# Optimization experiments

Measured on AMD Instinct MI355X. Metric: run time of the kernel, lower is better.

Reference implementation:

```python
import jax, jax.numpy as jnp
import numpy as np

B, N, DIM = 2, 2048, 2048
H, HD = 16, 128
EPS = 1e-5


def rmsnorm(x, w, eps=EPS):
    return x * jax.lax.rsqrt(jnp.mean(x * x, axis=-1, keepdims=True) + eps) * w


def rope(x, fr, fi):
    # x: [B, N, H, D]; fr/fi: [B, N, D//2] -> broadcast over heads
    x2 = x.reshape(*x.shape[:-1], HD // 2, 2)  # [B,N,H,D/2,2]
    x0, x1 = x2[..., 0], x2[..., 1]
    fr = fr[:, :, None, :]
    fi = fi[:, :, None, :]
    o0 = x0 * fr - x1 * fi
    o1 = x0 * fi + x1 * fr
    return jnp.stack([o0, o1], axis=-1).reshape(x.shape)


def setup_inputs() -> dict:
    key = jax.random.key(0)
    ks = jax.random.split(key, 7)
    s = 1.0 / np.sqrt(DIM)
    return {
        "x": jax.random.normal(ks[0], (B, N, DIM), jnp.float32),
        "freqs_real": jax.random.normal(ks[1], (B, N, HD // 2), jnp.float32),
        "freqs_imag": jax.random.normal(ks[2], (B, N, HD // 2), jnp.float32),
        "w_qkv": jax.random.normal(ks[3], (DIM, 3 * H * HD), jnp.float32) * s,
        "w_out": jax.random.normal(ks[4], (H * HD, DIM), jnp.float32) * s,
        "q_norm_w": jnp.ones((HD,), jnp.float32),
        "k_norm_w": jnp.ones((HD,), jnp.float32),
    }


def reference(x, freqs_real, freqs_imag, w_qkv, w_out, q_norm_w, k_norm_w):
    qkv = (x @ w_qkv).reshape(B, N, 3, H, HD)
    q, k, v = qkv[:, :, 0], qkv[:, :, 1], qkv[:, :, 2]  # [B,N,H,D]
    q = rmsnorm(q, q_norm_w)
    k = rmsnorm(k, k_norm_w)
    q = rope(q, freqs_real, freqs_imag)
    k = rope(k, freqs_real, freqs_imag)
    scale = 1.0 / np.sqrt(HD)
    scores = jnp.einsum("bqhd,bkhd->bhqk", q, k) * scale
    attn = jax.nn.softmax(scores, axis=-1)
    out = jnp.einsum("bhqk,bkhd->bqhd", attn, v).reshape(B, N, H * HD)
    return out @ w_out
```

## Files before the change

kernel.cpp:

```cpp
#include <hip/hip_runtime.h>
#include <hip/hip_bf16.h>
#include <stdint.h>

#define B_    2
#define N_    2048
#define DIM_  2048
#define H_    16
#define HD_   128
#define NH3   6144
#define ROWS  4096
#define EPS_  1e-5f

typedef unsigned short u16;
typedef __bf16 bf16x8 __attribute__((ext_vector_type(8)));
typedef float  f32x4  __attribute__((ext_vector_type(4)));

__device__ inline f32x4 mfma16(bf16x8 a, bf16x8 b, f32x4 c) {
  return __builtin_amdgcn_mfma_f32_16x16x32_bf16(a, b, c, 0, 0, 0);
}

__device__ inline u16 f2bf(float f) {
  union { float f; uint32_t u; } v; v.f = f;
  uint32_t u = v.u;
  return (u16)((u + 0x7fffu + ((u >> 16) & 1u)) >> 16);
}
__device__ inline float bf2f(u16 u) {
  union { uint32_t u; float f; } v; v.u = ((uint32_t)u) << 16;
  return v.f;
}

__device__ inline void gload_lds16(const void* g, void* l) {
  __builtin_amdgcn_global_load_lds(
      (const __attribute__((address_space(1))) void*)g,
      (__attribute__((address_space(3))) void*)l, 16, 0, 0);
}

__global__ __launch_bounds__(256) void cvt_f32_bf16(const float* __restrict__ in,
                                                    u16* __restrict__ out, int n) {
  int i = (blockIdx.x * 256 + threadIdx.x) * 4;
  if (i >= n) return;
  float4 v = *(const float4*)&in[i];
  ushort4 o;
  o.x = f2bf(v.x); o.y = f2bf(v.y); o.z = f2bf(v.z); o.w = f2bf(v.w);
  *(ushort4*)&out[i] = o;
}

__global__ __launch_bounds__(256) void transpose_cvt(const float* __restrict__ in,
                                                     u16* __restrict__ out,
                                                     int R, int C) {
  __shared__ float tile[32][33];
  int tc = blockIdx.x * 32, tr = blockIdx.y * 32;
  int tx = threadIdx.x, ty = threadIdx.y;
  #pragma unroll
  for (int i = 0; i < 4; ++i)
    tile[ty + i*8][tx] = in[(size_t)(tr + ty + i*8) * C + tc + tx];
  __syncthreads();
  #pragma unroll
  for (int i = 0; i < 4; ++i)
    out[(size_t)(tc + ty + i*8) * R + tr + tx] = f2bf(tile[tx][ty + i*8]);
}

__global__ __launch_bounds__(256) void v_transpose(const u16* __restrict__ qkv,
                                                   u16* __restrict__ vt) {
  __shared__ u16 lT[64][130];
  int bh = blockIdx.y, n0 = blockIdx.x * 64;
  int b = bh >> 4, h = bh & 15;
  int t = threadIdx.x;
  const u16* Vb = qkv + (size_t)b * N_ * NH3 + 4096 + h * HD_;
  #pragma unroll
  for (int i = 0; i < 16; ++i) {
    int chunk = i * 256 + t;
    int n = chunk >> 6, dc = chunk & 63;
    *(ushort2*)&lT[n][dc*2] = *(const ushort2*)&Vb[(size_t)(n0+n)*NH3 + dc*2];
  }
  __syncthreads();
  u16* vo = vt + (size_t)bh * HD_ * N_;
  #pragma unroll
  for (int i = 0; i < 4; ++i) {
    int chunk = i * 256 + t;
    int d = chunk >> 3, nc = chunk & 7;
    ushort4 a, bq;
    a.x = lT[nc*8+0][d]; a.y = lT[nc*8+1][d]; a.z = lT[nc*8+2][d]; a.w = lT[nc*8+3][d];
    bq.x = lT[nc*8+4][d]; bq.y = lT[nc*8+5][d]; bq.z = lT[nc*8+6][d]; bq.w = lT[nc*8+7][d];
    u16* dst = &vo[(size_t)d * N_ + n0 + nc*8];
    *(ushort4*)dst = a;
    *(ushort4*)(dst+4) = bq;
  }
}

template <bool OUT_BF16>
__global__ __launch_bounds__(256) void gemm_bt(const u16* __restrict__ A,
                                               const u16* __restrict__ Bt,
                                               void* __restrict__ Cv,
                                               int M, int N, int K) {
  __shared__ u16 lA[128][64];
  __shared__ u16 lB[128][64];
  int per = gridDim.x >> 3;
  int nid = (blockIdx.x & 7) * per + (blockIdx.x >> 3);
  int MB = M >> 7;
  int m0 = (nid % MB) * 128, n0 = (nid / MB) * 128;
  int t = threadIdx.x;
  int wave = t >> 6, lane = t & 63;
  int wr = wave >> 1, wc = wave & 1;
  int lhi = lane >> 4, llo = lane & 15;
  int lrow = lane >> 3, lcol = lane & 7;
  f32x4 acc[4][4] = {};

  for (int k0 = 0; k0 < K; k0 += 64) {
    __syncthreads();
    #pragma unroll
    for (int i = 0; i < 4; ++i) {
      int chunk = i * 4 + wave;
      int row = chunk * 8 + lrow;
      gload_lds16(&A[(size_t)(m0+row)*K + k0 + lcol*8], &lA[chunk*8][0]);
      gload_lds16(&Bt[(size_t)(n0+row)*K + k0 + lcol*8], &lB[chunk*8][0]);
    }
    __syncthreads();
    #pragma unroll
    for (int kk = 0; kk < 2; ++kk) {
      bf16x8 af[4], bfr[4];
      #pragma unroll
      for (int mi = 0; mi < 4; ++mi)
        af[mi] = *(const bf16x8*)&lA[wr*64 + mi*16 + llo][kk*32 + lhi*8];
      #pragma unroll
      for (int ni = 0; ni < 4; ++ni)
        bfr[ni] = *(const bf16x8*)&lB[wc*64 + ni*16 + llo][kk*32 + lhi*8];
      #pragma unroll
      for (int mi = 0; mi < 4; ++mi)
        #pragma unroll
        for (int ni = 0; ni < 4; ++ni)
          acc[mi][ni] = mfma16(af[mi], bfr[ni], acc[mi][ni]);
    }
  }
  #pragma unroll
  for (int mi = 0; mi < 4; ++mi)
    #pragma unroll
    for (int ni = 0; ni < 4; ++ni)
      #pragma unroll
      for (int r = 0; r < 4; ++r) {
        int row = m0 + wr*64 + mi*16 + lhi*4 + r;
        int col = n0 + wc*64 + ni*16 + llo;
        float v = acc[mi][ni][r];
        if constexpr (OUT_BF16) ((u16*)Cv)[(size_t)row*N + col] = f2bf(v);
        else                    ((float*)Cv)[(size_t)row*N + col] = v;
      }
}

__global__ __launch_bounds__(256) void norm_rope(u16* __restrict__ qkv,
                                                 const float* __restrict__ fr,
                                                 const float* __restrict__ fi,
                                                 const float* __restrict__ qw,
                                                 const float* __restrict__ kw) {
  int gw = (blockIdx.x * 256 + threadIdx.x) >> 6;
  int lane = threadIdx.x & 63;
  int row = gw >> 4, h = gw & 15;
  size_t base = (size_t)row * NH3 + h * HD_;
  ushort2 qp = *(ushort2*)&qkv[base + 2*lane];
  ushort2 kp = *(ushort2*)&qkv[base + 2048 + 2*lane];
  float q0 = bf2f(qp.x), q1 = bf2f(qp.y);
  float k0 = bf2f(kp.x), k1 = bf2f(kp.y);
  float sq = q0*q0 + q1*q1;
  float sk = k0*k0 + k1*k1;
  #pragma unroll
  for (int off = 1; off < 64; off <<= 1) {
    sq += __shfl_xor(sq, off);
    sk += __shfl_xor(sk, off);
  }
  float rq = rsqrtf(sq * (1.0f/128.0f) + EPS_);
  float rk = rsqrtf(sk * (1.0f/128.0f) + EPS_);
  float wq0 = qw[2*lane], wq1 = qw[2*lane+1];
  float wk0 = kw[2*lane], wk1 = kw[2*lane+1];
  q0 *= rq * wq0; q1 *= rq * wq1;
  k0 *= rk * wk0; k1 *= rk * wk1;
  float fre = fr[(size_t)row*64 + lane], fim = fi[(size_t)row*64 + lane];
  float qo0 = q0*fre - q1*fim, qo1 = q0*fim + q1*fre;
  float ko0 = k0*fre - k1*fim, ko1 = k0*fim + k1*fre;
  const float SC = 0.08838834764831845f;
  qo0 *= SC; qo1 *= SC;
  ushort2 qo, ko;
  qo.x = f2bf(qo0); qo.y = f2bf(qo1);
  ko.x = f2bf(ko0); ko.y = f2bf(ko1);
  *(ushort2*)&qkv[base + 2*lane] = qo;
  *(ushort2*)&qkv[base + 2048 + 2*lane] = ko;
}

__global__ __launch_bounds__(256) void attn(const u16* __restrict__ qkv,
                                            const u16* __restrict__ vt,
                                            u16* __restrict__ out) {
  int nid = (blockIdx.x & 7) * 64 + (blockIdx.x >> 3);
  int bh = nid >> 4;
  int b = bh >> 4, h = bh & 15;
  int q0 = (nid & 15) * 128;
  int t = threadIdx.x, wave = t >> 6, lane = t & 63;
  int lhi = lane >> 4, llo = lane & 15;

  __shared__ u16 lK[64][136];
  __shared__ u16 lVt[128][72];
  __shared__ u16 lP[4][32][72];

  const u16* Qb  = qkv + (size_t)b * N_ * NH3 + h * HD_;
  const u16* Kb  = Qb + 2048;
  const u16* Vtb = vt + (size_t)bh * HD_ * N_;

  bf16x8 qf[2][4];
  #pragma unroll
  for (int pi = 0; pi < 2; ++pi) {
    const u16* qrow = Qb + (size_t)(q0 + wave*32 + pi*16 + llo) * NH3;
    #pragma unroll
    for (int kk = 0; kk < 4; ++kk)
      qf[pi][kk] = *(const bf16x8*)&qrow[kk*32 + lhi*8];
  }

  f32x4 o[2][8] = {};
  float m_own[2] = {-1e30f, -1e30f};
  float l_own[2] = {0.f, 0.f};

  for (int kv0 = 0; kv0 < N_; kv0 += 64) {
    __syncthreads();
    #pragma unroll
    for (int i = 0; i < 4; ++i) {
      int chunk = i*256 + t;
      int row = chunk >> 4, kc = chunk & 15;
      *(int4*)&lK[row][kc*8] = *(const int4*)&Kb[(size_t)(kv0+row)*NH3 + kc*8];
    }
    #pragma unroll
    for (int i = 0; i < 4; ++i) {
      int chunk = i*256 + t;
      int d = chunk >> 3, kvc = chunk & 7;
      *(int4*)&lVt[d][kvc*8] = *(const int4*)&Vtb[(size_t)d*N_ + kv0 + kvc*8];
    }
    __syncthreads();

    f32x4 St[2][4];
    #pragma unroll
    for (int pi = 0; pi < 2; ++pi)
      #pragma unroll
      for (int j = 0; j < 4; ++j) St[pi][j] = f32x4{0.f,0.f,0.f,0.f};
    #pragma unroll
    for (int j = 0; j < 4; ++j)
      #pragma unroll
      for (int kk = 0; kk < 4; ++kk) {
        bf16x8 kf = *(const bf16x8*)&lK[j*16 + llo][kk*32 + lhi*8];
        St[0][j] = mfma16(kf, qf[0][kk], St[0][j]);
        St[1][j] = mfma16(kf, qf[1][kk], St[1][j]);
      }

    float scb[2][4];
    #pragma unroll
    for (int pi = 0; pi < 2; ++pi) {
      float mx = -1e30f;
      #pragma unroll
      for (int j = 0; j < 4; ++j) {
        float a = fmaxf(fmaxf(St[pi][j][0], St[pi][j][1]),
                        fmaxf(St[pi][j][2], St[pi][j][3]));
        mx = fmaxf(mx, a);
      }
      mx = fmaxf(mx, __shfl_xor(mx, 16));
      mx = fmaxf(mx, __shfl_xor(mx, 32));
      float mnew = fmaxf(m_own[pi], mx);
      float sc = __expf(m_own[pi] - mnew);
      m_own[pi] = mnew;
      float rs = 0.f;
      #pragma unroll
      for (int j = 0; j < 4; ++j)
        #pragma unroll
        for (int r = 0; r < 4; ++r) {
          float p = __expf(St[pi][j][r] - mnew);
          St[pi][j][r] = p;
          rs += p;
        }
      rs += __shfl_xor(rs, 16);
      rs += __shfl_xor(rs, 32);
      l_own[pi] = l_own[pi] * sc + rs;
      #pragma unroll
      for (int r = 0; r < 4; ++r) scb[pi][r] = __shfl(sc, lhi*4 + r, 16);
    }
    #pragma unroll
    for (int pi = 0; pi < 2; ++pi)
      #pragma unroll
      for (int d = 0; d < 8; ++d)
        #pragma unroll
        for (int r = 0; r < 4; ++r) o[pi][d][r] *= scb[pi][r];

    #pragma unroll
    for (int pi = 0; pi < 2; ++pi)
      #pragma unroll
      for (int j = 0; j < 4; ++j) {
        union { ushort4 u; __bf16 hv[4]; } pw;
        #pragma unroll
        for (int r = 0; r < 4; ++r) pw.hv[r] = (__bf16)St[pi][j][r];
        *(ushort4*)&lP[wave][pi*16 + llo][j*16 + lhi*4] = pw.u;
      }

    #pragma unroll
    for (int kk = 0; kk < 2; ++kk) {
      bf16x8 pf[2];
      #pragma unroll
      for (int pi = 0; pi < 2; ++pi)
        pf[pi] = *(const bf16x8*)&lP[wave][pi*16 + llo][kk*32 + lhi*8];
      #pragma unroll
      for (int d = 0; d < 8; ++d) {
        bf16x8 vf = *(const bf16x8*)&lVt[d*16 + llo][kk*32 + lhi*8];
        o[0][d] = mfma16(pf[0], vf, o[0][d]);
        o[1][d] = mfma16(pf[1], vf, o[1][d]);
      }
    }
  }

  float linv[2][4];
  #pragma unroll
  for (int pi = 0; pi < 2; ++pi)
    #pragma unroll
    for (int r = 0; r < 4; ++r)
      linv[pi][r] = 1.0f / __shfl(l_own[pi], lhi*4 + r, 16);
  #pragma unroll
  for (int pi = 0; pi < 2; ++pi)
    #pragma unroll
    for (int d = 0; d < 8; ++d)
      #pragma unroll
      for (int r = 0; r < 4; ++r) {
        size_t row = (size_t)b*N_ + q0 + wave*32 + pi*16 + lhi*4 + r;
        out[row*2048 + h*HD_ + d*16 + llo] = f2bf(o[pi][d][r] * linv[pi][r]);
      }
}

extern "C" void kernel_launch(void* const* d_in, const int* in_sizes, int n_in,
                              void* d_out, int out_size, void* d_ws, size_t ws_size,
                              hipStream_t stream) {
  const float* x    = (const float*)d_in[0];
  const float* fr   = (const float*)d_in[1];
  const float* fi   = (const float*)d_in[2];
  const float* wqkv = (const float*)d_in[3];
  const float* wout = (const float*)d_in[4];
  const float* qw   = (const float*)d_in[5];
  const float* kw   = (const float*)d_in[6];
  float* out = (float*)d_out;

  char* ws = (char*)d_ws;
  const size_t SZ_XB    = (size_t)ROWS * DIM_ * 2;
  const size_t SZ_WQKVT = (size_t)NH3  * DIM_ * 2;
  const size_t SZ_WOUTT = (size_t)DIM_ * DIM_ * 2;
  u16* xb    = (u16*)ws;
  u16* wqkvT = (u16*)(ws + SZ_XB);
  u16* woutT = (u16*)(ws + SZ_XB + SZ_WQKVT);
  u16* qkv   = (u16*)(ws + SZ_XB + SZ_WQKVT + SZ_WOUTT);
  u16* vtb   = xb;
  u16* attno = wqkvT;

  cvt_f32_bf16<<<(ROWS*DIM_/4 + 255)/256, 256, 0, stream>>>(x, xb, ROWS*DIM_);
  transpose_cvt<<<dim3(NH3/32, DIM_/32), dim3(32, 8), 0, stream>>>(wqkv, wqkvT, DIM_, NH3);
  transpose_cvt<<<dim3(DIM_/32, DIM_/32), dim3(32, 8), 0, stream>>>(wout, woutT, DIM_, DIM_);
  gemm_bt<true ><<<(ROWS/128)*(NH3/128), 256, 0, stream>>>(xb, wqkvT, qkv, ROWS, NH3, DIM_);
  norm_rope<<<ROWS*H_/4, 256, 0, stream>>>(qkv, fr, fi, qw, kw);
  v_transpose<<<dim3(N_/64, B_*H_), 256, 0, stream>>>(qkv, vtb);
  attn<<<(N_/128)*(B_*H_), 256, 0, stream>>>(qkv, vtb, attno);
  gemm_bt<false><<<(ROWS/128)*(DIM_/128), 256, 0, stream>>>(attno, woutT, out, ROWS, DIM_, DIM_);
}
```

Measured before the change: 551.6 us.

## Prefetch next K/V tile into registers and raise wave priority around MFMA

The attention kernel now loads the next 64-row K tile and V^T tile into registers while the current tile is being computed, then writes them to LDS at the top of the next iteration. This is meant to hide global-memory latency behind the QK and PV MFMA work. It also wraps the MFMA loops in s_setprio so matrix work gets scheduling priority. The cost is 8 extra int4 registers per thread, which may reduce occupancy.

```diff
diff --git a/kernel.cpp b/kernel.cpp
--- a/kernel.cpp
+++ b/kernel.cpp
@@ -211,31 +211,46 @@
       qf[pi][kk] = *(const bf16x8*)&qrow[kk*32 + lhi*8];
   }
 
+  int kc_row = t >> 4, kc_col = (t & 15) * 8;
+  int vc_row = t >> 3, vc_col = (t & 7) * 8;
+
   f32x4 o[2][8] = {};
   float m_own[2] = {-1e30f, -1e30f};
   float l_own[2] = {0.f, 0.f};
 
+  int4 kreg[4], vreg[4];
+  #pragma unroll
+  for (int i = 0; i < 4; ++i)
+    kreg[i] = *(const int4*)&Kb[(size_t)(i*16 + kc_row)*NH3 + kc_col];
+  #pragma unroll
+  for (int i = 0; i < 4; ++i)
+    vreg[i] = *(const int4*)&Vtb[(size_t)(i*32 + vc_row)*N_ + vc_col];
+
   for (int kv0 = 0; kv0 < N_; kv0 += 64) {
     __syncthreads();
     #pragma unroll
-    for (int i = 0; i < 4; ++i) {
-      int chunk = i*256 + t;
-      int row = chunk >> 4, kc = chunk & 15;
-      *(int4*)&lK[row][kc*8] = *(const int4*)&Kb[(size_t)(kv0+row)*NH3 + kc*8];
-    }
-    #pragma unroll
-    for (int i = 0; i < 4; ++i) {
-      int chunk = i*256 + t;
-      int d = chunk >> 3, kvc = chunk & 7;
-      *(int4*)&lVt[d][kvc*8] = *(const int4*)&Vtb[(size_t)d*N_ + kv0 + kvc*8];
-    }
+    for (int i = 0; i < 4; ++i)
+      *(int4*)&lK[i*16 + kc_row][kc_col] = kreg[i];
+    #pragma unroll
+    for (int i = 0; i < 4; ++i)
+      *(int4*)&lVt[i*32 + vc_row][vc_col] = vreg[i];
     __syncthreads();
 
+    if (kv0 + 64 < N_) {
+      #pragma unroll
+      for (int i = 0; i < 4; ++i)
+        kreg[i] = *(const int4*)&Kb[(size_t)(kv0 + 64 + i*16 + kc_row)*NH3 + kc_col];
+      #pragma unroll
+      for (int i = 0; i < 4; ++i)
+        vreg[i] = *(const int4*)&Vtb[(size_t)(i*32 + vc_row)*N_ + kv0 + 64 + vc_col];
+    }
+
     f32x4 St[2][4];
     #pragma unroll
     for (int pi = 0; pi < 2; ++pi)
       #pragma unroll
       for (int j = 0; j < 4; ++j) St[pi][j] = f32x4{0.f,0.f,0.f,0.f};
+    __builtin_amdgcn_s_setprio(1);
     #pragma unroll
     for (int j = 0; j < 4; ++j)
       #pragma unroll
@@ -244,6 +259,7 @@
         St[0][j] = mfma16(kf, qf[0][kk], St[0][j]);
         St[1][j] = mfma16(kf, qf[1][kk], St[1][j]);
       }
+    __builtin_amdgcn_s_setprio(0);
 
     float scb[2][4];
     #pragma unroll
@@ -292,6 +308,7 @@
         *(ushort4*)&lP[wave][pi*16 + llo][j*16 + lhi*4] = pw.u;
       }
 
+    __builtin_amdgcn_s_setprio(1);
     #pragma unroll
     for (int kk = 0; kk < 2; ++kk) {
       bf16x8 pf[2];
@@ -305,6 +322,7 @@
         o[1][d] = mfma16(pf[1], vf, o[1][d]);
       }
     }
+    __builtin_amdgcn_s_setprio(0);
   }
 
   float linv[2][4];
```

Result: slower. 619.7 us (+12.4%).

## Split attention work across eight waves with sixteen query rows each

Applied to the files above, without the earlier changes.

The attention kernel moves from 4 waves handling 32 query rows each to 8 waves (512 threads) handling 16 rows each, keeping the 128-row block tile. Per-thread accumulator and score registers are halved, and launch bounds request 4 blocks per CU, to raise occupancy and latency hiding. The trade-off is that each wave reuses every K/V fragment read from LDS for one MFMA instead of two, doubling LDS read traffic per FLOP, and block-wide barriers now synchronize more waves.

```diff
diff --git a/kernel.cpp b/kernel.cpp
--- a/kernel.cpp
+++ b/kernel.cpp
@@ -184,9 +184,9 @@
   *(ushort2*)&qkv[base + 2048 + 2*lane] = ko;
 }
 
-__global__ __launch_bounds__(256) void attn(const u16* __restrict__ qkv,
-                                            const u16* __restrict__ vt,
-                                            u16* __restrict__ out) {
+__global__ __launch_bounds__(512, 4) void attn(const u16* __restrict__ qkv,
+                                               const u16* __restrict__ vt,
+                                               u16* __restrict__ out) {
   int nid = (blockIdx.x & 7) * 64 + (blockIdx.x >> 3);
   int bh = nid >> 4;
   int b = bh >> 4, h = bh & 15;
@@ -196,132 +196,112 @@
 
   __shared__ u16 lK[64][136];
   __shared__ u16 lVt[128][72];
-  __shared__ u16 lP[4][32][72];
+  __shared__ u16 lP[8][16][72];
 
   const u16* Qb  = qkv + (size_t)b * N_ * NH3 + h * HD_;
   const u16* Kb  = Qb + 2048;
   const u16* Vtb = vt + (size_t)bh * HD_ * N_;
 
-  bf16x8 qf[2][4];
-  #pragma unroll
-  for (int pi = 0; pi < 2; ++pi) {
-    const u16* qrow = Qb + (size_t)(q0 + wave*32 + pi*16 + llo) * NH3;
+  bf16x8 qf[4];
+  {
+    const u16* qrow = Qb + (size_t)(q0 + wave*16 + llo) * NH3;
     #pragma unroll
     for (int kk = 0; kk < 4; ++kk)
-      qf[pi][kk] = *(const bf16x8*)&qrow[kk*32 + lhi*8];
-  }
-
-  f32x4 o[2][8] = {};
-  float m_own[2] = {-1e30f, -1e30f};
-  float l_own[2] = {0.f, 0.f};
+      qf[kk] = *(const bf16x8*)&qrow[kk*32 + lhi*8];
+  }
+
+  f32x4 o[8] = {};
+  float m_own = -1e30f;
+  float l_own = 0.f;
 
   for (int kv0 = 0; kv0 < N_; kv0 += 64) {
     __syncthreads();
     #pragma unroll
-    for (int i = 0; i < 4; ++i) {
-      int chunk = i*256 + t;
-      int row = chunk >> 4, kc = chunk & 15;
-      *(int4*)&lK[row][kc*8] = *(const int4*)&Kb[(size_t)(kv0+row)*NH3 + kc*8];
-    }
-    #pragma unroll
-    for (int i = 0; i < 4; ++i) {
-      int chunk = i*256 + t;
-      int d = chunk >> 3, kvc = chunk & 7;
-      *(int4*)&lVt[d][kvc*8] = *(const int4*)&Vtb[(size_t)d*N_ + kv0 + kvc*8];
+    for (int i = 0; i < 2; ++i) {
+      int c = i*512 + t;
+      int row = c >> 4, cc = (c & 15) * 8;
+      *(int4*)&lK[row][cc] = *(const int4*)&Kb[(size_t)(kv0+row)*NH3 + cc];
+    }
+    #pragma unroll
+    for (int i = 0; i < 2; ++i) {
+      int c = i*512 + t;
+      int d = c >> 3, cc = (c & 7) * 8;
+      *(int4*)&lVt[d][cc] = *(const int4*)&Vtb[(size_t)d*N_ + kv0 + cc];
     }
     __syncthreads();
 
-    f32x4 St[2][4];
-    #pragma unroll
-    for (int pi = 0; pi < 2; ++pi)
-      #pragma unroll
-      for (int j = 0; j < 4; ++j) St[pi][j] = f32x4{0.f,0.f,0.f,0.f};
+    f32x4 St[4];
+    #pragma unroll
+    for (int j = 0; j < 4; ++j) St[j] = f32x4{0.f,0.f,0.f,0.f};
     #pragma unroll
     for (int j = 0; j < 4; ++j)
       #pragma unroll
       for (int kk = 0; kk < 4; ++kk) {
         bf16x8 kf = *(const bf16x8*)&lK[j*16 + llo][kk*32 + lhi*8];
-        St[0][j] = mfma16(kf, qf[0][kk], St[0][j]);
-        St[1][j] = mfma16(kf, qf[1][kk], St[1][j]);
+        St[j] = mfma16(kf, qf[kk], St[j]);
       }
 
-    float scb[2][4];
-    #pragma unroll
-    for (int pi = 0; pi < 2; ++pi) {
-      float mx = -1e30f;
-      #pragma unroll
-      for (int j = 0; j < 4; ++j) {
-        float a = fmaxf(fmaxf(St[pi][j][0], St[pi][j][1]),
-                        fmaxf(St[pi][j][2], St[pi][j][3]));
-        mx = fmaxf(mx, a);
+    float mx = -1e30f;
+    #pragma unroll
+    for (int j = 0; j < 4; ++j) {
+      float a = fmaxf(fmaxf(St[j][0], St[j][1]), fmaxf(St[j][2], St[j][3]));
+      mx = fmaxf(mx, a);
+    }
+    mx = fmaxf(mx, __shfl_xor(mx, 16));
+    mx = fmaxf(mx, __shfl_xor(mx, 32));
+    float mnew = fmaxf(m_own, mx);
+    float sc = __expf(m_own - mnew);
+    m_own = mnew;
+    float rs = 0.f;
+    #pragma unroll
+    for (int j = 0; j < 4; ++j)
+      #pragma unroll
+      for (int r = 0; r < 4; ++r) {
+        float p = __expf(St[j][r] - mnew);
+        St[j][r] = p;
+        rs += p;
       }
-      mx = fmaxf(mx, __shfl_xor(mx, 16));
-      mx = fmaxf(mx, __shfl_xor(mx, 32));
-      float mnew = fmaxf(m_own[pi], mx);
-      float sc = __expf(m_own[pi] - mnew);
-      m_own[pi] = mnew;
-      float rs = 0.f;
-      #pragma unroll
-      for (int j = 0; j < 4; ++j)
-        #pragma unroll
-        for (int r = 0; r < 4; ++r) {
-          float p = __expf(St[pi][j][r] - mnew);
-          St[pi][j][r] = p;
-          rs += p;
-        }
-      rs += __shfl_xor(rs, 16);
-      rs += __shfl_xor(rs, 32);
-      l_own[pi] = l_own[pi] * sc + rs;
-      #pragma unroll
-      for (int r = 0; r < 4; ++r) scb[pi][r] = __shfl(sc, lhi*4 + r, 16);
-    }
-    #pragma unroll
-    for (int pi = 0; pi < 2; ++pi)
-      #pragma unroll
-      for (int d = 0; d < 8; ++d)
-        #pragma unroll
-        for (int r = 0; r < 4; ++r) o[pi][d][r] *= scb[pi][r];
-
-    #pragma unroll
-    for (int pi = 0; pi < 2; ++pi)
-      #pragma unroll
-      for (int j = 0; j < 4; ++j) {
-        union { ushort4 u; __bf16 hv[4]; } pw;
-        #pragma unroll
-        for (int r = 0; r < 4; ++r) pw.hv[r] = (__bf16)St[pi][j][r];
-        *(ushort4*)&lP[wave][pi*16 + llo][j*16 + lhi*4] = pw.u;
-      }
+    rs += __shfl_xor(rs, 16);
+    rs += __shfl_xor(rs, 32);
+    l_own = l_own * sc + rs;
+    float scb[4];
+    #pragma unroll
+    for (int r = 0; r < 4; ++r) scb[r] = __shfl(sc, lhi*4 + r, 16);
+    #pragma unroll
+    for (int d = 0; d < 8; ++d)
+      #pragma unroll
+      for (int r = 0; r < 4; ++r) o[d][r] *= scb[r];
+
+    #pragma unroll
+    for (int j = 0; j < 4; ++j) {
+      union { ushort4 u; __bf16 hv[4]; } pw;
+      #pragma unroll
+      for (int r = 0; r < 4; ++r) pw.hv[r] = (__bf16)St[j][r];
+      *(ushort4*)&lP[wave][llo][j*16 + lhi*4] = pw.u;
+    }
 
     #pragma unroll
     for (int kk = 0; kk < 2; ++kk) {
-      bf16x8 pf[2];
-      #pragma unroll
-      for (int pi = 0; pi < 2; ++pi)
-        pf[pi] = *(const bf16x8*)&lP[wave][pi*16 + llo][kk*32 + lhi*8];
+      bf16x8 pf = *(const bf16x8*)&lP[wave][llo][kk*32 + lhi*8];
       #pragma unroll
       for (int d = 0; d < 8; ++d) {
         bf16x8 vf = *(const bf16x8*)&lVt[d*16 + llo][kk*32 + lhi*8];
-        o[0][d] = mfma16(pf[0], vf, o[0][d]);
-        o[1][d] = mfma16(pf[1], vf, o[1][d]);
+        o[d] = mfma16(pf, vf, o[d]);
       }
     }
   }
 
-  float linv[2][4];
-  #pragma unroll
-  for (int pi = 0; pi < 2; ++pi)
-    #pragma unroll
-    for (int r = 0; r < 4; ++r)
-      linv[pi][r] = 1.0f / __shfl(l_own[pi], lhi*4 + r, 16);
-  #pragma unroll
-  for (int pi = 0; pi < 2; ++pi)
-    #pragma unroll
-    for (int d = 0; d < 8; ++d)
-      #pragma unroll
-      for (int r = 0; r < 4; ++r) {
-        size_t row = (size_t)b*N_ + q0 + wave*32 + pi*16 + lhi*4 + r;
-        out[row*2048 + h*HD_ + d*16 + llo] = f2bf(o[pi][d][r] * linv[pi][r]);
-      }
+  float linv[4];
+  #pragma unroll
+  for (int r = 0; r < 4; ++r)
+    linv[r] = 1.0f / __shfl(l_own, lhi*4 + r, 16);
+  #pragma unroll
+  for (int d = 0; d < 8; ++d)
+    #pragma unroll
+    for (int r = 0; r < 4; ++r) {
+      size_t row = (size_t)b*N_ + q0 + wave*16 + lhi*4 + r;
+      out[row*2048 + h*HD_ + d*16 + llo] = f2bf(o[d][r] * linv[r]);
+    }
 }
 
 extern "C" void kernel_launch(void* const* d_in, const int* in_sizes, int n_in,
@@ -353,6 +333,6 @@
   gemm_bt<true ><<<(ROWS/128)*(NH3/128), 256, 0, stream>>>(xb, wqkvT, qkv, ROWS, NH3, DIM_);
   norm_rope<<<ROWS*H_/4, 256, 0, stream>>>(qkv, fr, fi, qw, kw);
   v_transpose<<<dim3(N_/64, B_*H_), 256, 0, stream>>>(qkv, vtb);
-  attn<<<(N_/128)*(B_*H_), 256, 0, stream>>>(qkv, vtb, attno);
+  attn<<<(N_/128)*(B_*H_), 512, 0, stream>>>(qkv, vtb, attno);
   gemm_bt<false><<<(ROWS/128)*(DIM_/128), 256, 0, stream>>>(attno, woutT, out, ROWS, DIM_, DIM_);
 }
```

Measured after the change: 494.6 us. 10.3% less time.
